# Performance work log

Measured on AMD Instinct MI355X. Metric: run time of the kernel, lower is better.

The kernel has to match this reference:

```python
import jax, jax.numpy as jnp
import numpy as np

EPS_SN = 1e-12  # torch spectral_norm normalize eps
EPS_BN = 1e-5   # BatchNorm1d default eps


def _l2norm(x):
    return x / (jnp.linalg.norm(x) + EPS_SN)


def setup_inputs() -> dict:
    key = jax.random.key(0)
    ks = jax.random.split(key, 8)
    B, I, H, T = 4096, 64, 256, 64
    s_ih = 1.0 / np.sqrt(I)
    s_hh = 1.0 / np.sqrt(H)
    return {
        "inputs": jax.random.normal(ks[0], (B, I), dtype=jnp.float32),
        "w_ih": jax.random.uniform(ks[1], (3 * H, I), jnp.float32, -s_ih, s_ih),
        "w_hh": jax.random.uniform(ks[2], (3 * H, H), jnp.float32, -s_hh, s_hh),
        "b_ih": jax.random.uniform(ks[3], (3 * H,), jnp.float32, -s_hh, s_hh),
        "b_hh": jax.random.uniform(ks[4], (3 * H,), jnp.float32, -s_hh, s_hh),
        "w_lin": jax.random.uniform(ks[5], (I, H), jnp.float32, -s_hh, s_hh),
        "b_lin": jax.random.uniform(ks[6], (I,), jnp.float32, -s_hh, s_hh),
        "u_sn": jax.random.normal(ks[7], (I,), dtype=jnp.float32),
        "n_frames": T,
    }


def reference(inputs, w_ih, w_hh, b_ih, b_hh, w_lin, b_lin, u_sn, n_frames):
    H = w_hh.shape[1]
    B = inputs.shape[0]

    # spectral norm of linear weight: one power iteration, u/v detached (torch semantics)
    v = _l2norm(w_lin.T @ u_sn)
    u = _l2norm(w_lin @ v)
    sigma = jax.lax.stop_gradient(u) @ (w_lin @ jax.lax.stop_gradient(v))
    w_sn = w_lin / sigma

    h0 = jnp.zeros((B, H), dtype=inputs.dtype)

    def step(carry, _):
        h, x = carry
        gi = x @ w_ih.T + b_ih          # [B, 3H]
        gh = h @ w_hh.T + b_hh          # [B, 3H]
        i_r, i_z, i_n = jnp.split(gi, 3, axis=-1)
        h_r, h_z, h_n = jnp.split(gh, 3, axis=-1)
        r = jax.nn.sigmoid(i_r + h_r)
        z = jax.nn.sigmoid(i_z + h_z)
        n = jnp.tanh(i_n + r * h_n)
        h_new = (1.0 - z) * n + z * h
        y = h_new @ w_sn.T + b_lin      # fed back as next input
        return (h_new, y), y

    _, outs = jax.lax.scan(step, (h0, inputs), None, length=n_frames)  # [T, B, O]

    # BatchNorm1d(affine=False), training mode: per-timestep batch stats (biased var)
    mean = jnp.mean(outs, axis=1, keepdims=True)
    var = jnp.mean(jnp.square(outs - mean), axis=1, keepdims=True)
    return (outs - mean) / jnp.sqrt(var + EPS_BN)
```

## Files before the change

### kernel.cpp

```cpp
#include <hip/hip_runtime.h>
#include <hip/hip_bf16.h>


typedef __attribute__((ext_vector_type(8))) short short8;
typedef __attribute__((ext_vector_type(4))) float f32x4;
typedef __hip_bfloat16 bf16_t;

#define BATCH 4096
#define ISZ 64
#define HSZ 256
#define TSZ 64

__device__ __forceinline__ float sigm(float x) { return 1.f / (1.f + __expf(-x)); }
__device__ __forceinline__ float tanh_fast(float x) { return 1.f - 2.f / (1.f + __expf(2.f * x)); }

__device__ __forceinline__ void load_cvt(const float* __restrict__ p, short8& a0, short8& a1) {
  f32x4 u = *reinterpret_cast<const f32x4*>(p);
  f32x4 w = *reinterpret_cast<const f32x4*>(p + 4);
  float x[8] = {u[0], u[1], u[2], u[3], w[0], w[1], w[2], w[3]};
#pragma unroll
  for (int e = 0; e < 8; ++e) {
    bf16_t h0 = __float2bfloat16(x[e]);
    a0[e] = *reinterpret_cast<short*>(&h0);
    bf16_t h1 = __float2bfloat16(x[e] - __bfloat162float(h0));
    a1[e] = *reinterpret_cast<short*>(&h1);
  }
}

__device__ __forceinline__ void async16(const void* g, void* l) {
  __builtin_amdgcn_global_load_lds(
      (const __attribute__((address_space(1))) unsigned int*)g,
      (__attribute__((address_space(3))) unsigned int*)l, 16, 0, 0);
}

__global__ __launch_bounds__(256) void prep_sn(
    const float* __restrict__ w_lin, const float* __restrict__ u_sn,
    double* __restrict__ w_sn_f64)
{
  __shared__ double v[HSZ];
  __shared__ double red[256];
  __shared__ double Wv[ISZ];
  int t = threadIdx.x;
  double s = 0.0;
  for (int i = 0; i < ISZ; ++i) s += (double)w_lin[i * HSZ + t] * (double)u_sn[i];
  red[t] = s * s;
  __syncthreads();
  for (int off = 128; off > 0; off >>= 1) { if (t < off) red[t] += red[t + off]; __syncthreads(); }
  double nv = sqrt(red[0]);
  v[t] = s / (nv + 1e-12);
  __syncthreads();
  {
    int i = t >> 2, p = t & 3;
    double ps = 0.0;
    for (int k = p * 64; k < p * 64 + 64; ++k) ps += (double)w_lin[i * HSZ + k] * v[k];
    red[t] = ps;
    __syncthreads();
    if ((t & 3) == 0) Wv[i] = red[t] + red[t + 1] + red[t + 2] + red[t + 3];
    __syncthreads();
  }
  red[t] = (t < ISZ) ? Wv[t] * Wv[t] : 0.0;
  __syncthreads();
  for (int off = 128; off > 0; off >>= 1) { if (t < off) red[t] += red[t + off]; __syncthreads(); }
  double nw = sqrt(red[0]);
  double sigma = red[0] / (nw + 1e-12);
  double inv_sigma = 1.0 / sigma;
  for (int idx = t; idx < ISZ * HSZ; idx += 256)
    w_sn_f64[idx] = (double)w_lin[idx] * inv_sigma;
}

__global__ __launch_bounds__(256) void split2_f32(
    const float* __restrict__ x, bf16_t* __restrict__ p0, bf16_t* __restrict__ p1, int n)
{
  int i = blockIdx.x * 256 + threadIdx.x;
  if (i < n) {
    float v = x[i];
    bf16_t a = __float2bfloat16(v);
    p0[i] = a;
    p1[i] = __float2bfloat16(v - __bfloat162float(a));
  }
}

__global__ __launch_bounds__(256) void split2_f64(
    const double* __restrict__ x, bf16_t* __restrict__ p0, bf16_t* __restrict__ p1, int n)
{
  int i = blockIdx.x * 256 + threadIdx.x;
  if (i < n) {
    double v = x[i];
    bf16_t a = __float2bfloat16((float)v);
    p0[i] = a;
    p1[i] = __float2bfloat16((float)(v - (double)__bfloat162float(a)));
  }
}

__global__ __launch_bounds__(256) void gru_first(
    const bf16_t* __restrict__ X0, const bf16_t* __restrict__ X1,
    const bf16_t* __restrict__ Wi0, const bf16_t* __restrict__ Wi1,
    const float* __restrict__ b_ih, const float* __restrict__ b_hh,
    float* __restrict__ hF)
{
  const int jb = blockIdx.y;
  const int mw = blockIdx.x * 128 + (threadIdx.x >> 6) * 32;
  const int l = threadIdx.x & 63;
  const int lr = l & 15;
  const int lq = l >> 4;
  const int j = jb * 16 + lr;

  f32x4 accM[2][3], accC[2][3];
#pragma unroll
  for (int mt = 0; mt < 2; ++mt)
#pragma unroll
    for (int g = 0; g < 3; ++g) {
      accM[mt][g] = (f32x4){0.f, 0.f, 0.f, 0.f};
      accC[mt][g] = (f32x4){0.f, 0.f, 0.f, 0.f};
    }

#pragma unroll
  for (int kk = 0; kk < ISZ; kk += 32) {
    short8 a0[2], a1[2];
#pragma unroll
    for (int mt = 0; mt < 2; ++mt) {
      size_t ao = (size_t)(mw + mt * 16 + lr) * ISZ + kk + lq * 8;
      a0[mt] = *reinterpret_cast<const short8*>(X0 + ao);
      a1[mt] = *reinterpret_cast<const short8*>(X1 + ao);
    }
#pragma unroll
    for (int g = 0; g < 3; ++g) {
      size_t bo = (size_t)(g * HSZ + jb * 16 + lr) * ISZ + kk + lq * 8;
      short8 b0 = *reinterpret_cast<const short8*>(Wi0 + bo);
      short8 b1 = *reinterpret_cast<const short8*>(Wi1 + bo);
#pragma unroll
      for (int mt = 0; mt < 2; ++mt) {
        accC[mt][g] = __builtin_amdgcn_mfma_f32_16x16x32_bf16(a0[mt], b1, accC[mt][g], 0, 0, 0);
        accC[mt][g] = __builtin_amdgcn_mfma_f32_16x16x32_bf16(a1[mt], b0, accC[mt][g], 0, 0, 0);
        accM[mt][g] = __builtin_amdgcn_mfma_f32_16x16x32_bf16(a0[mt], b0, accM[mt][g], 0, 0, 0);
      }
    }
  }

  const float brz = b_ih[j] + b_hh[j];
  const float bzz = b_ih[HSZ + j] + b_hh[HSZ + j];
  const float bin = b_ih[2 * HSZ + j];
  const float bhn = b_hh[2 * HSZ + j];

#pragma unroll
  for (int mt = 0; mt < 2; ++mt) {
#pragma unroll
    for (int q = 0; q < 4; ++q) {
      int b = mw + mt * 16 + lq * 4 + q;
      float r = sigm(accM[mt][0][q] + accC[mt][0][q] + brz);
      float z = sigm(accM[mt][1][q] + accC[mt][1][q] + bzz);
      float n = tanh_fast(accM[mt][2][q] + accC[mt][2][q] + bin + r * bhn);
      hF[(size_t)b * HSZ + j] = (1.f - z) * n;
    }
  }
}

__global__ __launch_bounds__(256) void gru_gates(
    const float* __restrict__ yprev,
    const float* __restrict__ hF,
    const bf16_t* __restrict__ Wi0, const bf16_t* __restrict__ Wi1,
    const bf16_t* __restrict__ Wh0, const bf16_t* __restrict__ Wh1,
    const float* __restrict__ b_ih, const float* __restrict__ b_hh,
    float* __restrict__ hFo)
{
  __shared__ __align__(16) short lWh[96 * 256];
  __shared__ __align__(16) short lWi[96 * 64];

  const int jb = blockIdx.y;
  const int tid = threadIdx.x;
  const int wid = tid >> 6;
  const int mw = blockIdx.x * 128 + wid * 32;
  const int l = tid & 63;
  const int lr = l & 15;
  const int lq = l >> 4;
  const int j = jb * 16 + lr;

#pragma unroll
  for (int i = 0; i < 12; ++i) {
    int L = i * 4096 + tid * 16;
    int R = L >> 9, c16 = L & 511;
    int csrc = c16 ^ ((R & 7) << 4);
    int g = R >> 5, p = (R >> 4) & 1, jr = R & 15;
    const bf16_t* srcrow = (p ? Wh1 : Wh0) + (size_t)(g * HSZ + jb * 16 + jr) * HSZ;
    async16((const char*)srcrow + csrc, (char*)lWh + i * 4096 + wid * 1024);
  }
#pragma unroll
  for (int i = 0; i < 3; ++i) {
    int L = i * 4096 + tid * 16;
    int R = L >> 7, c16 = L & 127;
    int csrc = c16 ^ ((R & 7) << 4);
    int g = R >> 5, p = (R >> 4) & 1, jr = R & 15;
    const bf16_t* srcrow = (p ? Wi1 : Wi0) + (size_t)(g * HSZ + jb * 16 + jr) * ISZ;
    async16((const char*)srcrow + csrc, (char*)lWi + i * 4096 + wid * 1024);
  }

  float hold_[2][4];
#pragma unroll
  for (int mt = 0; mt < 2; ++mt)
#pragma unroll
    for (int q = 0; q < 4; ++q)
      hold_[mt][q] = hF[(size_t)(mw + mt * 16 + lq * 4 + q) * HSZ + j];

  asm volatile("s_waitcnt vmcnt(0)" ::: "memory");
  __syncthreads();

  f32x4 accM[2][4], accC[2][4];
#pragma unroll
  for (int mt = 0; mt < 2; ++mt)
#pragma unroll
    for (int g = 0; g < 4; ++g) {
      accM[mt][g] = (f32x4){0.f, 0.f, 0.f, 0.f};
      accC[mt][g] = (f32x4){0.f, 0.f, 0.f, 0.f};
    }

  auto whf = [&](int g, int p, int c) -> short8 {
    int R = (g * 2 + p) * 16 + lr;
    int byte = R * 512 + ((c * 64 + lq * 16) ^ ((lr & 7) << 4));
    return *reinterpret_cast<const short8*>((const char*)lWh + byte);
  };
  auto wif = [&](int g, int p, int c) -> short8 {
    int R = (g * 2 + p) * 16 + lr;
    int byte = R * 128 + ((c * 64 + lq * 16) ^ ((lr & 7) << 4));
    return *reinterpret_cast<const short8*>((const char*)lWi + byte);
  };

#pragma unroll
  for (int c = 0; c < 2; ++c) {
    short8 a0[2], a1[2];
#pragma unroll
    for (int mt = 0; mt < 2; ++mt)
      load_cvt(yprev + (size_t)(mw + mt * 16 + lr) * ISZ + c * 32 + lq * 8, a0[mt], a1[mt]);
#pragma unroll
    for (int g = 0; g < 3; ++g) {
      short8 b0 = wif(g, 0, c);
      short8 b1 = wif(g, 1, c);
#pragma unroll
      for (int mt = 0; mt < 2; ++mt) {
        accC[mt][g] = __builtin_amdgcn_mfma_f32_16x16x32_bf16(a0[mt], b1, accC[mt][g], 0, 0, 0);
        accC[mt][g] = __builtin_amdgcn_mfma_f32_16x16x32_bf16(a1[mt], b0, accC[mt][g], 0, 0, 0);
        accM[mt][g] = __builtin_amdgcn_mfma_f32_16x16x32_bf16(a0[mt], b0, accM[mt][g], 0, 0, 0);
      }
    }
  }

#pragma unroll
  for (int c = 0; c < 8; ++c) {
    short8 a0[2], a1[2];
#pragma unroll
    for (int mt = 0; mt < 2; ++mt)
      load_cvt(hF + (size_t)(mw + mt * 16 + lr) * HSZ + c * 32 + lq * 8, a0[mt], a1[mt]);
#pragma unroll
    for (int g = 0; g < 3; ++g) {
      const int tgt = (g == 2) ? 3 : g;
      short8 b0 = whf(g, 0, c);
      short8 b1 = whf(g, 1, c);
#pragma unroll
      for (int mt = 0; mt < 2; ++mt) {
        accC[mt][tgt] = __builtin_amdgcn_mfma_f32_16x16x32_bf16(a0[mt], b1, accC[mt][tgt], 0, 0, 0);
        accC[mt][tgt] = __builtin_amdgcn_mfma_f32_16x16x32_bf16(a1[mt], b0, accC[mt][tgt], 0, 0, 0);
        accM[mt][tgt] = __builtin_amdgcn_mfma_f32_16x16x32_bf16(a0[mt], b0, accM[mt][tgt], 0, 0, 0);
      }
    }
  }

  const float brz = b_ih[j] + b_hh[j];
  const float bzz = b_ih[HSZ + j] + b_hh[HSZ + j];
  const float bin = b_ih[2 * HSZ + j];
  const float bhn = b_hh[2 * HSZ + j];

#pragma unroll
  for (int mt = 0; mt < 2; ++mt) {
#pragma unroll
    for (int q = 0; q < 4; ++q) {
      int b = mw + mt * 16 + lq * 4 + q;
      float rpre = accM[mt][0][q] + accC[mt][0][q] + brz;
      float zpre = accM[mt][1][q] + accC[mt][1][q] + bzz;
      float inn  = accM[mt][2][q] + accC[mt][2][q] + bin;
      float hnn  = accM[mt][3][q] + accC[mt][3][q] + bhn;
      float r = sigm(rpre);
      float z = sigm(zpre);
      float n = tanh_fast(inn + r * hnn);
      double hv = (double)((1.f - z) * n) + (double)z * (double)hold_[mt][q];
      hFo[(size_t)b * HSZ + j] = (float)hv;
    }
  }
}

__global__ __launch_bounds__(64) void y_step(
    const float* __restrict__ hF,
    const bf16_t* __restrict__ Ws0, const bf16_t* __restrict__ Ws1,
    const float* __restrict__ b_lin,
    float* __restrict__ yout)
{
  const int mw = blockIdx.x * 16;
  const int nt = blockIdx.y;
  const int l = threadIdx.x;
  const int lr = l & 15;
  const int lq = l >> 4;

  f32x4 accM = (f32x4){0.f, 0.f, 0.f, 0.f};
  f32x4 accC = (f32x4){0.f, 0.f, 0.f, 0.f};

  for (int kk = 0; kk < HSZ; kk += 32) {
    short8 a0, a1;
    load_cvt(hF + (size_t)(mw + lr) * HSZ + kk + lq * 8, a0, a1);
    size_t bo = (size_t)(nt * 16 + lr) * HSZ + kk + lq * 8;
    short8 b0 = *reinterpret_cast<const short8*>(Ws0 + bo);
    short8 b1 = *reinterpret_cast<const short8*>(Ws1 + bo);
    accC = __builtin_amdgcn_mfma_f32_16x16x32_bf16(a0, b1, accC, 0, 0, 0);
    accC = __builtin_amdgcn_mfma_f32_16x16x32_bf16(a1, b0, accC, 0, 0, 0);
    accM = __builtin_amdgcn_mfma_f32_16x16x32_bf16(a0, b0, accM, 0, 0, 0);
  }

  const int o = nt * 16 + lr;
  const float bl = b_lin[o];
#pragma unroll
  for (int q = 0; q < 4; ++q) {
    size_t row = mw + lq * 4 + q;
    yout[row * 64 + o] = accM[q] + accC[q] + bl;
  }
}

__global__ __launch_bounds__(256) void bn_part(const float* __restrict__ Y,
                                               double* __restrict__ psum,
                                               double* __restrict__ psum2)
{
  int t = blockIdx.x;
  int chunk = blockIdx.y;
  int o = threadIdx.x & 63, rg = threadIdx.x >> 6;
  const float* Yt = Y + (size_t)t * BATCH * 64;
  int b0 = chunk * 256;
  double s = 0.0, s2 = 0.0;
  for (int b = b0 + rg; b < b0 + 256; b += 4) {
    double v = (double)Yt[(size_t)b * 64 + o];
    s += v;
    s2 += v * v;
  }
  __shared__ double ls[4][64], ls2[4][64];
  ls[rg][o] = s;
  ls2[rg][o] = s2;
  __syncthreads();
  if (rg == 0) {
    s = ls[0][o] + ls[1][o] + ls[2][o] + ls[3][o];
    s2 = ls2[0][o] + ls2[1][o] + ls2[2][o] + ls2[3][o];
    size_t pi = ((size_t)t * 16 + chunk) * 64 + o;
    psum[pi] = s;
    psum2[pi] = s2;
  }
}

__global__ __launch_bounds__(64) void bn_final(const double* __restrict__ psum,
                                               const double* __restrict__ psum2,
                                               float* __restrict__ mean,
                                               float* __restrict__ istd)
{
  int t = blockIdx.x;
  int o = threadIdx.x;
  double s = 0.0, s2 = 0.0;
  for (int c = 0; c < 16; ++c) {
    size_t pi = ((size_t)t * 16 + c) * 64 + o;
    s += psum[pi];
    s2 += psum2[pi];
  }
  double m = s * (1.0 / BATCH);
  double var = s2 * (1.0 / BATCH) - m * m;
  mean[t * 64 + o] = (float)m;
  istd[t * 64 + o] = (float)(1.0 / sqrt(var + 1e-5));
}

__global__ __launch_bounds__(256) void bn_norm(float* __restrict__ Y,
                                               const float* __restrict__ mean,
                                               const float* __restrict__ istd, int n4)
{
  for (int i = blockIdx.x * 256 + threadIdx.x; i < n4; i += gridDim.x * 256) {
    f32x4 v = reinterpret_cast<f32x4*>(Y)[i];
    int base = i * 4;
    int o = base & 63;
    int t = base >> 18;
    const float* mr = mean + t * 64;
    const float* ir = istd + t * 64;
#pragma unroll
    for (int e = 0; e < 4; ++e) v[e] = (v[e] - mr[o + e]) * ir[o + e];
    reinterpret_cast<f32x4*>(Y)[i] = v;
  }
}

extern "C" void kernel_launch(void* const* d_in, const int* in_sizes, int n_in,
                              void* d_out, int out_size, void* d_ws, size_t ws_size,
                              hipStream_t stream)
{
  const float* inputs = (const float*)d_in[0];
  const float* w_ih = (const float*)d_in[1];
  const float* w_hh = (const float*)d_in[2];
  const float* b_ih = (const float*)d_in[3];
  const float* b_hh = (const float*)d_in[4];
  const float* w_lin = (const float*)d_in[5];
  const float* b_lin = (const float*)d_in[6];
  const float* u_sn = (const float*)d_in[7];
  float* out = (float*)d_out;

  const size_t BH = (size_t)BATCH * HSZ;
  const size_t BI = (size_t)BATCH * ISZ;

  char* ws = (char*)d_ws;
  size_t off = 0;
  auto alloc = [&](size_t bytes) -> void* {
    void* p = ws + off;
    off += (bytes + 255) & ~(size_t)255;
    return p;
  };
  double* w_sn_f64 = (double*)alloc((size_t)ISZ * HSZ * 8);
  bf16_t* Wi0 = (bf16_t*)alloc((size_t)3 * HSZ * ISZ * 2);
  bf16_t* Wi1 = (bf16_t*)alloc((size_t)3 * HSZ * ISZ * 2);
  bf16_t* Wh0 = (bf16_t*)alloc((size_t)3 * HSZ * HSZ * 2);
  bf16_t* Wh1 = (bf16_t*)alloc((size_t)3 * HSZ * HSZ * 2);
  bf16_t* Ws0 = (bf16_t*)alloc((size_t)ISZ * HSZ * 2);
  bf16_t* Ws1 = (bf16_t*)alloc((size_t)ISZ * HSZ * 2);
  bf16_t* X0 = (bf16_t*)alloc(BI * 2);
  bf16_t* X1 = (bf16_t*)alloc(BI * 2);
  float* hFA = (float*)alloc(BH * 4);
  float* hFB = (float*)alloc(BH * 4);
  double* psum = (double*)alloc((size_t)TSZ * 16 * 64 * 8);
  double* psum2 = (double*)alloc((size_t)TSZ * 16 * 64 * 8);
  float* meanb = (float*)alloc(TSZ * 64 * 4);
  float* istdb = (float*)alloc(TSZ * 64 * 4);
  if (off > ws_size) return;

  prep_sn<<<1, 256, 0, stream>>>(w_lin, u_sn, w_sn_f64);
  split2_f32<<<(3 * HSZ * ISZ + 255) / 256, 256, 0, stream>>>(w_ih, Wi0, Wi1, 3 * HSZ * ISZ);
  split2_f32<<<(3 * HSZ * HSZ + 255) / 256, 256, 0, stream>>>(w_hh, Wh0, Wh1, 3 * HSZ * HSZ);
  split2_f64<<<(ISZ * HSZ + 255) / 256, 256, 0, stream>>>(w_sn_f64, Ws0, Ws1, ISZ * HSZ);
  split2_f32<<<((int)BI + 255) / 256, 256, 0, stream>>>(inputs, X0, X1, (int)BI);

  gru_first<<<dim3(BATCH / 128, 16), 256, 0, stream>>>(X0, X1, Wi0, Wi1, b_ih, b_hh, hFA);
  y_step<<<dim3(BATCH / 16, 4), 64, 0, stream>>>(hFA, Ws0, Ws1, b_lin, out);

  float* hin = hFA;
  float* hout = hFB;
  for (int t = 1; t < TSZ; ++t) {
    gru_gates<<<dim3(BATCH / 128, 16), 256, 0, stream>>>(
        out + (size_t)(t - 1) * BATCH * 64, hin,
        Wi0, Wi1, Wh0, Wh1, b_ih, b_hh, hout);
    y_step<<<dim3(BATCH / 16, 4), 64, 0, stream>>>(hout, Ws0, Ws1, b_lin,
                                                   out + (size_t)t * BATCH * 64);
    float* tm = hin; hin = hout; hout = tm;
  }

  bn_part<<<dim3(TSZ, 16), 256, 0, stream>>>(out, psum, psum2);
  bn_final<<<TSZ, 64, 0, stream>>>(psum, psum2, meanb, istdb);
  bn_norm<<<2048, 256, 0, stream>>>(out, meanb, istdb, TSZ * BATCH * 64 / 4);
}
```

Baseline: 1.456 ms.

## Fuse output projection into GRU step kernel, recomputing y per hidden tile

Removes the separate y_step launch per timestep. Each gru_step_f block computes y = h_prev @ Ws^T + b_lin from the h tile it already loads, stores it (jb==0 writes to global), splits it to bf16 pairs in LDS, and uses it for the input-gate GEMM. This halves kernel launches and drops the y round trip through global memory. In exchange the y projection is recomputed redundantly by all 16 column blocks, with Ws read from global without LDS staging, and LDS use grows.

```diff
diff --git a/kernel.cpp b/kernel.cpp
--- a/kernel.cpp
+++ b/kernel.cpp
@@ -155,16 +155,17 @@
   }
 }
 
-__global__ __launch_bounds__(256) void gru_gates(
-    const float* __restrict__ yprev,
+__global__ __launch_bounds__(256) void gru_step_f(
     const float* __restrict__ hF,
     const bf16_t* __restrict__ Wi0, const bf16_t* __restrict__ Wi1,
     const bf16_t* __restrict__ Wh0, const bf16_t* __restrict__ Wh1,
+    const bf16_t* __restrict__ Ws0, const bf16_t* __restrict__ Ws1,
     const float* __restrict__ b_ih, const float* __restrict__ b_hh,
-    float* __restrict__ hFo)
-{
-  __shared__ __align__(16) short lWh[96 * 256];
-  __shared__ __align__(16) short lWi[96 * 64];
+    const float* __restrict__ b_lin,
+    float* __restrict__ hFo,
+    float* __restrict__ yout)
+{
+  __shared__ __align__(16) short lds[38912];
 
   const int jb = blockIdx.y;
   const int tid = threadIdx.x;
@@ -182,7 +183,7 @@
     int csrc = c16 ^ ((R & 7) << 4);
     int g = R >> 5, p = (R >> 4) & 1, jr = R & 15;
     const bf16_t* srcrow = (p ? Wh1 : Wh0) + (size_t)(g * HSZ + jb * 16 + jr) * HSZ;
-    async16((const char*)srcrow + csrc, (char*)lWh + i * 4096 + wid * 1024);
+    async16((const char*)srcrow + csrc, (char*)lds + i * 4096 + wid * 1024);
   }
 #pragma unroll
   for (int i = 0; i < 3; ++i) {
@@ -191,7 +192,7 @@
     int csrc = c16 ^ ((R & 7) << 4);
     int g = R >> 5, p = (R >> 4) & 1, jr = R & 15;
     const bf16_t* srcrow = (p ? Wi1 : Wi0) + (size_t)(g * HSZ + jb * 16 + jr) * ISZ;
-    async16((const char*)srcrow + csrc, (char*)lWi + i * 4096 + wid * 1024);
+    async16((const char*)srcrow + csrc, (char*)lds + 49152 + i * 4096 + wid * 1024);
   }
 
   float hold_[2][4];
@@ -204,44 +205,31 @@
   asm volatile("s_waitcnt vmcnt(0)" ::: "memory");
   __syncthreads();
 
-  f32x4 accM[2][4], accC[2][4];
-#pragma unroll
-  for (int mt = 0; mt < 2; ++mt)
-#pragma unroll
-    for (int g = 0; g < 4; ++g) {
-      accM[mt][g] = (f32x4){0.f, 0.f, 0.f, 0.f};
-      accC[mt][g] = (f32x4){0.f, 0.f, 0.f, 0.f};
-    }
+  f32x4 gM[2][3], gC[2][3], yM[2][4], yC[2][4];
+#pragma unroll
+  for (int mt = 0; mt < 2; ++mt) {
+#pragma unroll
+    for (int g = 0; g < 3; ++g) {
+      gM[mt][g] = (f32x4){0.f, 0.f, 0.f, 0.f};
+      gC[mt][g] = (f32x4){0.f, 0.f, 0.f, 0.f};
+    }
+#pragma unroll
+    for (int nt = 0; nt < 4; ++nt) {
+      yM[mt][nt] = (f32x4){0.f, 0.f, 0.f, 0.f};
+      yC[mt][nt] = (f32x4){0.f, 0.f, 0.f, 0.f};
+    }
+  }
 
   auto whf = [&](int g, int p, int c) -> short8 {
     int R = (g * 2 + p) * 16 + lr;
     int byte = R * 512 + ((c * 64 + lq * 16) ^ ((lr & 7) << 4));
-    return *reinterpret_cast<const short8*>((const char*)lWh + byte);
+    return *reinterpret_cast<const short8*>((const char*)lds + byte);
   };
   auto wif = [&](int g, int p, int c) -> short8 {
     int R = (g * 2 + p) * 16 + lr;
-    int byte = R * 128 + ((c * 64 + lq * 16) ^ ((lr & 7) << 4));
-    return *reinterpret_cast<const short8*>((const char*)lWi + byte);
+    int byte = 49152 + R * 128 + ((c * 64 + lq * 16) ^ ((lr & 7) << 4));
+    return *reinterpret_cast<const short8*>((const char*)lds + byte);
   };
-
-#pragma unroll
-  for (int c = 0; c < 2; ++c) {
-    short8 a0[2], a1[2];
-#pragma unroll
-    for (int mt = 0; mt < 2; ++mt)
-      load_cvt(yprev + (size_t)(mw + mt * 16 + lr) * ISZ + c * 32 + lq * 8, a0[mt], a1[mt]);
-#pragma unroll
-    for (int g = 0; g < 3; ++g) {
-      short8 b0 = wif(g, 0, c);
-      short8 b1 = wif(g, 1, c);
-#pragma unroll
-      for (int mt = 0; mt < 2; ++mt) {
-        accC[mt][g] = __builtin_amdgcn_mfma_f32_16x16x32_bf16(a0[mt], b1, accC[mt][g], 0, 0, 0);
-        accC[mt][g] = __builtin_amdgcn_mfma_f32_16x16x32_bf16(a1[mt], b0, accC[mt][g], 0, 0, 0);
-        accM[mt][g] = __builtin_amdgcn_mfma_f32_16x16x32_bf16(a0[mt], b0, accM[mt][g], 0, 0, 0);
-      }
-    }
-  }
 
 #pragma unroll
   for (int c = 0; c < 8; ++c) {
@@ -251,14 +239,25 @@
       load_cvt(hF + (size_t)(mw + mt * 16 + lr) * HSZ + c * 32 + lq * 8, a0[mt], a1[mt]);
 #pragma unroll
     for (int g = 0; g < 3; ++g) {
-      const int tgt = (g == 2) ? 3 : g;
       short8 b0 = whf(g, 0, c);
       short8 b1 = whf(g, 1, c);
 #pragma unroll
       for (int mt = 0; mt < 2; ++mt) {
-        accC[mt][tgt] = __builtin_amdgcn_mfma_f32_16x16x32_bf16(a0[mt], b1, accC[mt][tgt], 0, 0, 0);
-        accC[mt][tgt] = __builtin_amdgcn_mfma_f32_16x16x32_bf16(a1[mt], b0, accC[mt][tgt], 0, 0, 0);
-        accM[mt][tgt] = __builtin_amdgcn_mfma_f32_16x16x32_bf16(a0[mt], b0, accM[mt][tgt], 0, 0, 0);
+        gC[mt][g] = __builtin_amdgcn_mfma_f32_16x16x32_bf16(a0[mt], b1, gC[mt][g], 0, 0, 0);
+        gC[mt][g] = __builtin_amdgcn_mfma_f32_16x16x32_bf16(a1[mt], b0, gC[mt][g], 0, 0, 0);
+        gM[mt][g] = __builtin_amdgcn_mfma_f32_16x16x32_bf16(a0[mt], b0, gM[mt][g], 0, 0, 0);
+      }
+    }
+#pragma unroll
+    for (int nt = 0; nt < 4; ++nt) {
+      size_t bo = (size_t)(nt * 16 + lr) * HSZ + c * 32 + lq * 8;
+      short8 b0 = *reinterpret_cast<const short8*>(Ws0 + bo);
+      short8 b1 = *reinterpret_cast<const short8*>(Ws1 + bo);
+#pragma unroll
+      for (int mt = 0; mt < 2; ++mt) {
+        yC[mt][nt] = __builtin_amdgcn_mfma_f32_16x16x32_bf16(a0[mt], b1, yC[mt][nt], 0, 0, 0);
+        yC[mt][nt] = __builtin_amdgcn_mfma_f32_16x16x32_bf16(a1[mt], b0, yC[mt][nt], 0, 0, 0);
+        yM[mt][nt] = __builtin_amdgcn_mfma_f32_16x16x32_bf16(a0[mt], b0, yM[mt][nt], 0, 0, 0);
       }
     }
   }
@@ -267,16 +266,57 @@
   const float bzz = b_ih[HSZ + j] + b_hh[HSZ + j];
   const float bin = b_ih[2 * HSZ + j];
   const float bhn = b_hh[2 * HSZ + j];
+  float bl[4];
+#pragma unroll
+  for (int nt = 0; nt < 4; ++nt) bl[nt] = b_lin[nt * 16 + lr];
+
+  char* xbase = (char*)lds + 61440 + wid * 4096;
 
 #pragma unroll
   for (int mt = 0; mt < 2; ++mt) {
+#pragma unroll
+    for (int q = 0; q < 4; ++q) {
+      int row16 = lq * 4 + q;
+      int sw = (row16 & 7) << 4;
+#pragma unroll
+      for (int nt = 0; nt < 4; ++nt) {
+        int col = nt * 16 + lr;
+        float yf = yM[mt][nt][q] + yC[mt][nt][q] + bl[nt];
+        if (jb == 0) yout[(size_t)(mw + mt * 16 + row16) * 64 + col] = yf;
+        bf16_t p0 = __float2bfloat16(yf);
+        bf16_t p1 = __float2bfloat16(yf - __bfloat162float(p0));
+        int bo2 = row16 * 128 + ((2 * col) ^ sw);
+        *(short*)(xbase + bo2) = *reinterpret_cast<short*>(&p0);
+        *(short*)(xbase + 2048 + bo2) = *reinterpret_cast<short*>(&p1);
+      }
+    }
+    f32x4 iM[3], iC[3];
+#pragma unroll
+    for (int g = 0; g < 3; ++g) {
+      iM[g] = (f32x4){0.f, 0.f, 0.f, 0.f};
+      iC[g] = (f32x4){0.f, 0.f, 0.f, 0.f};
+    }
+#pragma unroll
+    for (int c = 0; c < 2; ++c) {
+      int rb = lr * 128 + ((c * 64 + lq * 16) ^ ((lr & 7) << 4));
+      short8 a0 = *reinterpret_cast<const short8*>(xbase + rb);
+      short8 a1 = *reinterpret_cast<const short8*>(xbase + 2048 + rb);
+#pragma unroll
+      for (int g = 0; g < 3; ++g) {
+        short8 b0 = wif(g, 0, c);
+        short8 b1 = wif(g, 1, c);
+        iC[g] = __builtin_amdgcn_mfma_f32_16x16x32_bf16(a0, b1, iC[g], 0, 0, 0);
+        iC[g] = __builtin_amdgcn_mfma_f32_16x16x32_bf16(a1, b0, iC[g], 0, 0, 0);
+        iM[g] = __builtin_amdgcn_mfma_f32_16x16x32_bf16(a0, b0, iM[g], 0, 0, 0);
+      }
+    }
 #pragma unroll
     for (int q = 0; q < 4; ++q) {
       int b = mw + mt * 16 + lq * 4 + q;
-      float rpre = accM[mt][0][q] + accC[mt][0][q] + brz;
-      float zpre = accM[mt][1][q] + accC[mt][1][q] + bzz;
-      float inn  = accM[mt][2][q] + accC[mt][2][q] + bin;
-      float hnn  = accM[mt][3][q] + accC[mt][3][q] + bhn;
+      float rpre = iM[0][q] + iC[0][q] + gM[mt][0][q] + gC[mt][0][q] + brz;
+      float zpre = iM[1][q] + iC[1][q] + gM[mt][1][q] + gC[mt][1][q] + bzz;
+      float inn  = iM[2][q] + iC[2][q] + bin;
+      float hnn  = gM[mt][2][q] + gC[mt][2][q] + bhn;
       float r = sigm(rpre);
       float z = sigm(zpre);
       float n = tanh_fast(inn + r * hnn);
@@ -433,18 +473,17 @@
   split2_f32<<<((int)BI + 255) / 256, 256, 0, stream>>>(inputs, X0, X1, (int)BI);
 
   gru_first<<<dim3(BATCH / 128, 16), 256, 0, stream>>>(X0, X1, Wi0, Wi1, b_ih, b_hh, hFA);
-  y_step<<<dim3(BATCH / 16, 4), 64, 0, stream>>>(hFA, Ws0, Ws1, b_lin, out);
 
   float* hin = hFA;
   float* hout = hFB;
   for (int t = 1; t < TSZ; ++t) {
-    gru_gates<<<dim3(BATCH / 128, 16), 256, 0, stream>>>(
-        out + (size_t)(t - 1) * BATCH * 64, hin,
-        Wi0, Wi1, Wh0, Wh1, b_ih, b_hh, hout);
-    y_step<<<dim3(BATCH / 16, 4), 64, 0, stream>>>(hout, Ws0, Ws1, b_lin,
-                                                   out + (size_t)t * BATCH * 64);
+    gru_step_f<<<dim3(BATCH / 128, 16), 256, 0, stream>>>(
+        hin, Wi0, Wi1, Wh0, Wh1, Ws0, Ws1, b_ih, b_hh, b_lin,
+        hout, out + (size_t)(t - 1) * BATCH * 64);
     float* tm = hin; hin = hout; hout = tm;
   }
+  y_step<<<dim3(BATCH / 16, 4), 64, 0, stream>>>(hin, Ws0, Ws1, b_lin,
+                                                 out + (size_t)(TSZ - 1) * BATCH * 64);
 
   bn_part<<<dim3(TSZ, 16), 256, 0, stream>>>(out, psum, psum2);
   bn_final<<<TSZ, 64, 0, stream>>>(psum, psum2, meanb, istdb);
```

New measurement: 2.055 ms. 41.1% more time.
